# Kernel optimization log

Measured on AMD Instinct MI355X. Metric: run time of the kernel, lower is better.

Reference implementation:

```python
import jax, jax.numpy as jnp
import numpy as np

N = 50000      # nodes
E = 800000     # edges
D_IN = 128
D_H = 128
D_OUT = 40
BN_EPS = 1e-5


def setup_inputs() -> dict:
    key = jax.random.key(0)
    ks = jax.random.split(key, 12)
    x = jax.random.normal(ks[0], (N, D_IN), dtype=jnp.float32)
    edge_index = jax.random.randint(ks[1], (2, E), 0, N, dtype=jnp.int32)
    s = 0.05
    W1 = jax.random.normal(ks[2], (D_IN, D_H), dtype=jnp.float32) * s
    b1 = jnp.zeros((D_H,), jnp.float32)
    W2 = jax.random.normal(ks[3], (D_H, D_H), dtype=jnp.float32) * s
    b2 = jnp.zeros((D_H,), jnp.float32)
    W3 = jax.random.normal(ks[4], (D_H, D_OUT), dtype=jnp.float32) * s
    b3 = jnp.zeros((D_OUT,), jnp.float32)
    # BatchNorm (eval mode: running stats)
    g1 = jnp.ones((D_H,), jnp.float32)
    be1 = jnp.zeros((D_H,), jnp.float32)
    m1 = jax.random.normal(ks[5], (D_H,), dtype=jnp.float32) * 0.1
    v1 = jax.random.uniform(ks[6], (D_H,), dtype=jnp.float32, minval=0.5, maxval=1.5)
    g2 = jnp.ones((D_H,), jnp.float32)
    be2 = jnp.zeros((D_H,), jnp.float32)
    m2 = jax.random.normal(ks[7], (D_H,), dtype=jnp.float32) * 0.1
    v2 = jax.random.uniform(ks[8], (D_H,), dtype=jnp.float32, minval=0.5, maxval=1.5)
    return {"x": x, "edge_index": edge_index,
            "W1": W1, "b1": b1, "W2": W2, "b2": b2, "W3": W3, "b3": b3,
            "g1": g1, "be1": be1, "m1": m1, "v1": v1,
            "g2": g2, "be2": be2, "m2": m2, "v2": v2}


def gcn_conv(x, W, b, src, dst):
    # PyG GCNConv: h = x W; A_hat = D^-1/2 (A + I) D^-1/2; out = A_hat h + b
    h = x @ W                                   # [N, d_out]
    deg = jnp.zeros((N,), h.dtype).at[dst].add(1.0) + 1.0   # degrees incl. self loop
    dis = jax.lax.rsqrt(deg)                    # deg^-1/2
    norm = dis[src] * dis[dst]                  # [E]
    msg = h[src] * norm[:, None]                # [E, d_out] gather + scale
    agg = jax.ops.segment_sum(msg, dst, num_segments=N)     # scatter-add
    agg = agg + h * (1.0 / deg)[:, None]        # self-loop term: dis_i*dis_i = 1/deg_i
    return agg + b


def bn_eval(x, gamma, beta, mean, var):
    return (x - mean) * jax.lax.rsqrt(var + BN_EPS) * gamma + beta


def reference(x, edge_index, W1, b1, W2, b2, W3, b3,
              g1, be1, m1, v1, g2, be2, m2, v2):
    src, dst = edge_index[0], edge_index[1]
    h = jax.nn.relu(bn_eval(gcn_conv(x, W1, b1, src, dst), g1, be1, m1, v1))
    h = jax.nn.relu(bn_eval(gcn_conv(h, W2, b2, src, dst), g2, be2, m2, v2))
    h = gcn_conv(h, W3, b3, src, dst)
    return jax.nn.log_softmax(h, axis=-1)
```

## Files before the change

kernel.cpp:

```cpp
#include <hip/hip_runtime.h>
#include <math.h>

#define BN_EPS 1e-5f

typedef __attribute__((ext_vector_type(8))) short bf16x8;
typedef __attribute__((ext_vector_type(4))) float f32x4;

__device__ inline unsigned f2bf(float f) {
  union { float f; unsigned u; } v; v.f = f;
  unsigned r = v.u + 0x7FFF + ((v.u >> 16) & 1);
  return r >> 16;
}

__device__ inline void acc8n(float* a, uint4 v) {
  a[0] += __uint_as_float(v.x << 16);
  a[1] += __uint_as_float(v.x & 0xffff0000u);
  a[2] += __uint_as_float(v.y << 16);
  a[3] += __uint_as_float(v.y & 0xffff0000u);
  a[4] += __uint_as_float(v.z << 16);
  a[5] += __uint_as_float(v.z & 0xffff0000u);
  a[6] += __uint_as_float(v.w << 16);
  a[7] += __uint_as_float(v.w & 0xffff0000u);
}

__device__ inline void acc4n(float* a, uint2 v) {
  a[0] += __uint_as_float(v.x << 16);
  a[1] += __uint_as_float(v.x & 0xffff0000u);
  a[2] += __uint_as_float(v.y << 16);
  a[3] += __uint_as_float(v.y & 0xffff0000u);
}


__global__ void k_count(const int* __restrict__ dst, int* __restrict__ deg,
                        int* __restrict__ posw, int E) {
  int e = blockIdx.x * blockDim.x + threadIdx.x;
  if (e < E) posw[e] = atomicAdd(&deg[dst[e]], 1);
}

__global__ void k_scan1(const int* __restrict__ deg, int* __restrict__ rowstart,
                        int* __restrict__ chunksum, int n) {
  __shared__ int s[1024];
  int i = blockIdx.x * 1024 + threadIdx.x;
  int v = (i < n) ? deg[i] : 0;
  s[threadIdx.x] = v;
  __syncthreads();
  for (int off = 1; off < 1024; off <<= 1) {
    int t = (threadIdx.x >= off) ? s[threadIdx.x - off] : 0;
    __syncthreads();
    s[threadIdx.x] += t;
    __syncthreads();
  }
  if (i < n) rowstart[i] = s[threadIdx.x] - v;
  if (threadIdx.x == 1023) chunksum[blockIdx.x] = s[1023];
}

__global__ void k_scan3(int* __restrict__ rowstart, const int* __restrict__ chunksum,
                        const int* __restrict__ deg, float* __restrict__ dis,
                        int n, int E) {
  int pre = 0;
  for (int c = 0; c < (int)blockIdx.x; c++) pre += chunksum[c];
  int i = blockIdx.x * 1024 + threadIdx.x;
  if (i < n) {
    rowstart[i] += pre;
    dis[i] = rsqrtf((float)(deg[i] + 1));
  }
  if (i == 0) rowstart[n] = E;
}


__global__ void k_prep(const float* __restrict__ W1, const float* __restrict__ W2,
                       const float* __restrict__ W3,
                       const float* __restrict__ g1, const float* __restrict__ be1,
                       const float* __restrict__ m1, const float* __restrict__ v1,
                       const float* __restrict__ g2, const float* __restrict__ be2,
                       const float* __restrict__ m2, const float* __restrict__ v2,
                       const float* __restrict__ b1, const float* __restrict__ b2,
                       const float* __restrict__ b3,
                       ushort* __restrict__ WT1, ushort* __restrict__ WT2,
                       ushort* __restrict__ WT3,
                       float* __restrict__ sc1, float* __restrict__ sh1,
                       float* __restrict__ sc2, float* __restrict__ sh2,
                       float* __restrict__ b3pad,
                       uint4* __restrict__ degz, int deg16) {
  int k = blockIdx.x;
  int n = threadIdx.x;
  int tid = k * 128 + n;
  if (tid < deg16) degz[tid] = make_uint4(0, 0, 0, 0);
  WT1[n * 128 + k] = (ushort)f2bf(W1[k * 128 + n]);
  WT2[n * 128 + k] = (ushort)f2bf(W2[k * 128 + n]);
  WT3[n * 128 + k] = (n < 40) ? (ushort)f2bf(W3[k * 40 + n]) : (ushort)0;
  if (k == 0) {
    float s1 = g1[n] * rsqrtf(v1[n] + BN_EPS);
    sc1[n] = s1; sh1[n] = be1[n] + (b1[n] - m1[n]) * s1;
    float s2 = g2[n] * rsqrtf(v2[n] + BN_EPS);
    sc2[n] = s2; sh2[n] = be2[n] + (b2[n] - m2[n]) * s2;
  } else if (k == 1 && n < 64) {
    b3pad[n] = (n < 40) ? b3[n] : 0.f;
  }
}


template <bool F32A, bool FILL>
__global__ __launch_bounds__(256) void k_gemm_bf16(const void* __restrict__ Ap,
                                                   const ushort* __restrict__ WT,
                                                   ushort* __restrict__ C,
                                                   const float* __restrict__ dis,
                                                   int nrows, int NC, int gemmBlocks,
                                                   const int* __restrict__ ei,
                                                   const int* __restrict__ rowstart,
                                                   const int* __restrict__ posw,
                                                   unsigned* __restrict__ slot, int E) {
  if (FILL && (int)blockIdx.x >= gemmBlocks) {
    int e = ((int)blockIdx.x - gemmBlocks) * 256 + threadIdx.x;
    if (e < E) slot[rowstart[ei[E + e]] + posw[e]] = (unsigned)ei[e];
    return;
  }
  __shared__ ushort As[128][80];
  __shared__ ushort Bs[128][80];
  const int tid  = threadIdx.x;
  const int lane = tid & 63;
  const int wid  = tid >> 6;
  const int wr   = wid >> 1, wc = wid & 1;
  const int row0 = blockIdx.x * 128;
  f32x4 acc[4][4] = {};

  const int mrow = lane & 15;
  const int kg   = (lane >> 4) * 8;

  for (int k0 = 0; k0 < 128; k0 += 64) {
    __syncthreads();
    for (int i = tid; i < 1024; i += 256) {
      int r = i >> 3, c = (i & 7) * 8;
      uint4 w = make_uint4(0, 0, 0, 0);
      if (row0 + r < nrows) {
        if (F32A) {
          const float* A = (const float*)Ap;
          float4 v0 = *(const float4*)(A + (size_t)(row0 + r) * 128 + k0 + c);
          float4 v1 = *(const float4*)(A + (size_t)(row0 + r) * 128 + k0 + c + 4);
          w.x = f2bf(v0.x) | (f2bf(v0.y) << 16);
          w.y = f2bf(v0.z) | (f2bf(v0.w) << 16);
          w.z = f2bf(v1.x) | (f2bf(v1.y) << 16);
          w.w = f2bf(v1.z) | (f2bf(v1.w) << 16);
        } else {
          const ushort* A = (const ushort*)Ap;
          w = *(const uint4*)(A + (size_t)(row0 + r) * 128 + k0 + c);
        }
      }
      *(uint4*)(&As[r][c]) = w;
    }
    for (int i = tid; i < 1024; i += 256) {
      int r = i >> 3, c = (i & 7) * 8;
      *(uint4*)(&Bs[r][c]) = *(const uint4*)(WT + r * 128 + k0 + c);
    }
    __syncthreads();

#pragma unroll
    for (int ks = 0; ks < 2; ks++) {
      bf16x8 a[4], b[4];
#pragma unroll
      for (int f = 0; f < 4; f++) {
        a[f] = *(const bf16x8*)(&As[wr * 64 + f * 16 + mrow][ks * 32 + kg]);
        b[f] = *(const bf16x8*)(&Bs[wc * 64 + f * 16 + mrow][ks * 32 + kg]);
      }
#pragma unroll
      for (int fm = 0; fm < 4; fm++)
#pragma unroll
        for (int fn = 0; fn < 4; fn++)
          acc[fm][fn] = __builtin_amdgcn_mfma_f32_16x16x32_bf16(a[fm], b[fn], acc[fm][fn], 0, 0, 0);
    }
  }

  const int rl = (lane >> 4) * 4;
  const int cl = lane & 15;
#pragma unroll
  for (int fm = 0; fm < 4; fm++) {
#pragma unroll
    for (int r = 0; r < 4; r++) {
      int row = row0 + wr * 64 + fm * 16 + rl + r;
      if (row >= nrows) continue;
      float dn = dis[row];
#pragma unroll
      for (int fn = 0; fn < 4; fn++) {
        int col = wc * 64 + fn * 16 + cl;
        if (col < NC) C[(size_t)row * NC + col] = (ushort)f2bf(acc[fm][fn][r] * dn);
      }
    }
  }
}


__global__ __launch_bounds__(256) void k_agg128b(const ushort* __restrict__ h,
                          const int* __restrict__ rowstart,
                          const unsigned* __restrict__ slot,
                          const float* __restrict__ dis,
                          const float* __restrict__ bnsc,
                          const float* __restrict__ bnsh,
                          ushort* __restrict__ out, int nnodes) {
  int node = blockIdx.x * 4 + threadIdx.y;
  if (node >= nnodes) return;
  int lane = threadIdx.x;
  int eg = lane >> 4, cl = lane & 15, c0 = cl * 8;
  int s = rowstart[node], e = rowstart[node + 1];
  int deg = e - s;
  unsigned mys = 0;
  if (lane < deg) mys = slot[s + lane];
  float a[8] = {0.f, 0.f, 0.f, 0.f, 0.f, 0.f, 0.f, 0.f};
  int nb = deg < 64 ? deg : 64;
  int i = eg;
  for (; i + 12 < nb; i += 16) {
    int s0 = __shfl((int)mys, i);
    int s1 = __shfl((int)mys, i + 4);
    int s2 = __shfl((int)mys, i + 8);
    int s3 = __shfl((int)mys, i + 12);
    uint4 h0 = *(const uint4*)(h + (size_t)s0 * 128 + c0);
    uint4 h1 = *(const uint4*)(h + (size_t)s1 * 128 + c0);
    uint4 h2 = *(const uint4*)(h + (size_t)s2 * 128 + c0);
    uint4 h3 = *(const uint4*)(h + (size_t)s3 * 128 + c0);
    acc8n(a, h0); acc8n(a, h1); acc8n(a, h2); acc8n(a, h3);
  }
  for (; i + 4 < nb; i += 8) {
    int s0 = __shfl((int)mys, i);
    int s1 = __shfl((int)mys, i + 4);
    uint4 h0 = *(const uint4*)(h + (size_t)s0 * 128 + c0);
    uint4 h1 = *(const uint4*)(h + (size_t)s1 * 128 + c0);
    acc8n(a, h0); acc8n(a, h1);
  }
  if (i < nb) {
    int s0 = __shfl((int)mys, i);
    uint4 h0 = *(const uint4*)(h + (size_t)s0 * 128 + c0);
    acc8n(a, h0);
  }
  for (int j = s + 64 + eg; j < e; j += 4) {
    uint4 h0 = *(const uint4*)(h + (size_t)slot[j] * 128 + c0);
    acc8n(a, h0);
  }
#pragma unroll
  for (int j = 0; j < 8; j++) {
    a[j] += __shfl_xor(a[j], 16);
    a[j] += __shfl_xor(a[j], 32);
  }
  if (eg == 0) {
    uint4 hv = *(const uint4*)(h + (size_t)node * 128 + c0);
    acc8n(a, hv);
    float dn = dis[node];
    float4 sc0 = *(const float4*)(bnsc + c0), sc1 = *(const float4*)(bnsc + c0 + 4);
    float4 sh0 = *(const float4*)(bnsh + c0), sh1 = *(const float4*)(bnsh + c0 + 4);
    float o0 = fmaxf(fmaf(a[0] * dn, sc0.x, sh0.x), 0.f);
    float o1 = fmaxf(fmaf(a[1] * dn, sc0.y, sh0.y), 0.f);
    float o2 = fmaxf(fmaf(a[2] * dn, sc0.z, sh0.z), 0.f);
    float o3 = fmaxf(fmaf(a[3] * dn, sc0.w, sh0.w), 0.f);
    float o4 = fmaxf(fmaf(a[4] * dn, sc1.x, sh1.x), 0.f);
    float o5 = fmaxf(fmaf(a[5] * dn, sc1.y, sh1.y), 0.f);
    float o6 = fmaxf(fmaf(a[6] * dn, sc1.z, sh1.z), 0.f);
    float o7 = fmaxf(fmaf(a[7] * dn, sc1.w, sh1.w), 0.f);
    uint4 w;
    w.x = f2bf(o0) | (f2bf(o1) << 16);
    w.y = f2bf(o2) | (f2bf(o3) << 16);
    w.z = f2bf(o4) | (f2bf(o5) << 16);
    w.w = f2bf(o6) | (f2bf(o7) << 16);
    *(uint4*)(out + (size_t)node * 128 + c0) = w;
  }
}


__global__ __launch_bounds__(256) void k_agg64_lsm(const ushort* __restrict__ h,
                            const int* __restrict__ rowstart,
                            const unsigned* __restrict__ slot,
                            const float* __restrict__ dis,
                            const float* __restrict__ b3pad,
                            float* __restrict__ out, int nnodes) {
  int node = blockIdx.x * 4 + threadIdx.y;
  if (node >= nnodes) return;
  int lane = threadIdx.x;
  int eg = lane >> 4, cl = lane & 15, c0 = cl * 4;
  int s = rowstart[node], e = rowstart[node + 1];
  int deg = e - s;
  unsigned mys = 0;
  if (lane < deg) mys = slot[s + lane];
  float a[4] = {0.f, 0.f, 0.f, 0.f};
  int nb = deg < 64 ? deg : 64;
  int i = eg;
  for (; i + 12 < nb; i += 16) {
    int s0 = __shfl((int)mys, i);
    int s1 = __shfl((int)mys, i + 4);
    int s2 = __shfl((int)mys, i + 8);
    int s3 = __shfl((int)mys, i + 12);
    uint2 h0 = *(const uint2*)(h + (size_t)s0 * 64 + c0);
    uint2 h1 = *(const uint2*)(h + (size_t)s1 * 64 + c0);
    uint2 h2 = *(const uint2*)(h + (size_t)s2 * 64 + c0);
    uint2 h3 = *(const uint2*)(h + (size_t)s3 * 64 + c0);
    acc4n(a, h0); acc4n(a, h1); acc4n(a, h2); acc4n(a, h3);
  }
  for (; i + 4 < nb; i += 8) {
    int s0 = __shfl((int)mys, i);
    int s1 = __shfl((int)mys, i + 4);
    uint2 h0 = *(const uint2*)(h + (size_t)s0 * 64 + c0);
    uint2 h1 = *(const uint2*)(h + (size_t)s1 * 64 + c0);
    acc4n(a, h0); acc4n(a, h1);
  }
  if (i < nb) {
    int s0 = __shfl((int)mys, i);
    uint2 h0 = *(const uint2*)(h + (size_t)s0 * 64 + c0);
    acc4n(a, h0);
  }
  for (int j = s + 64 + eg; j < e; j += 4) {
    uint2 h0 = *(const uint2*)(h + (size_t)slot[j] * 64 + c0);
    acc4n(a, h0);
  }
#pragma unroll
  for (int j = 0; j < 4; j++) {
    a[j] += __shfl_xor(a[j], 16);
    a[j] += __shfl_xor(a[j], 32);
  }
  {
    uint2 hv = *(const uint2*)(h + (size_t)node * 64 + c0);
    acc4n(a, hv);
    float dn = dis[node];
    float4 bb = *(const float4*)(b3pad + c0);
    a[0] = fmaf(a[0], dn, bb.x);
    a[1] = fmaf(a[1], dn, bb.y);
    a[2] = fmaf(a[2], dn, bb.z);
    a[3] = fmaf(a[3], dn, bb.w);
  }
  bool valid = cl < 10;
  float m = valid ? fmaxf(fmaxf(a[0], a[1]), fmaxf(a[2], a[3])) : -INFINITY;
#pragma unroll
  for (int off = 1; off < 16; off <<= 1) m = fmaxf(m, __shfl_xor(m, off));
  float ss = valid ? (expf(a[0] - m) + expf(a[1] - m) + expf(a[2] - m) + expf(a[3] - m)) : 0.f;
#pragma unroll
  for (int off = 1; off < 16; off <<= 1) ss += __shfl_xor(ss, off);
  float lse = m + logf(ss);
  if (eg == 0 && valid) {
    *(float4*)(out + (size_t)node * 40 + c0) =
        make_float4(a[0] - lse, a[1] - lse, a[2] - lse, a[3] - lse);
  }
}


extern "C" void kernel_launch(void* const* d_in, const int* in_sizes, int n_in,
                              void* d_out, int out_size, void* d_ws, size_t ws_size,
                              hipStream_t stream) {
  const float* x   = (const float*)d_in[0];
  const int*   ei  = (const int*)d_in[1];
  const float* W1  = (const float*)d_in[2];
  const float* b1  = (const float*)d_in[3];
  const float* W2  = (const float*)d_in[4];
  const float* b2  = (const float*)d_in[5];
  const float* W3  = (const float*)d_in[6];
  const float* b3  = (const float*)d_in[7];
  const float* g1  = (const float*)d_in[8];
  const float* be1 = (const float*)d_in[9];
  const float* m1  = (const float*)d_in[10];
  const float* v1  = (const float*)d_in[11];
  const float* g2  = (const float*)d_in[12];
  const float* be2 = (const float*)d_in[13];
  const float* m2  = (const float*)d_in[14];
  const float* v2  = (const float*)d_in[15];

  const int N   = in_sizes[0] / 128;
  const int E   = in_sizes[1] / 2;

  float* outp = (float*)d_out;

  char* ws = (char*)d_ws;
  size_t off = 0;
  auto alloc = [&](size_t bytes) -> char* {
    char* p = ws + off;
    off = (off + bytes + 255) & ~(size_t)255;
    return p;
  };
  const int deg16 = (N + 3) / 4;
  int*      deg      = (int*)alloc((size_t)deg16 * 16);
  int*      posw     = (int*)alloc((size_t)E * 4);
  int*      rowstart = (int*)alloc((size_t)(N + 1) * 4);
  int*      chunksum = (int*)alloc(256 * 4);
  float*    dis      = (float*)alloc((size_t)N * 4);
  unsigned* slot     = (unsigned*)alloc((size_t)E * 4);
  float*    sc1      = (float*)alloc(128 * 4);
  float*    sh1      = (float*)alloc(128 * 4);
  float*    sc2      = (float*)alloc(128 * 4);
  float*    sh2      = (float*)alloc(128 * 4);
  float*    b3pad    = (float*)alloc(64 * 4);
  ushort*   WT1      = (ushort*)alloc(128 * 128 * 2);
  ushort*   WT2      = (ushort*)alloc(128 * 128 * 2);
  ushort*   WT3      = (ushort*)alloc(128 * 128 * 2);
  ushort*   bufA     = (ushort*)alloc((size_t)N * 128 * 2);
  ushort*   bufB     = (ushort*)alloc((size_t)N * 128 * 2);
  ushort*   bufC     = (ushort*)alloc((size_t)N * 64 * 2);
  (void)ws_size;

  const int T = 256;
  const int chunks = (N + 1023) / 1024;

  k_prep<<<128, 128, 0, stream>>>(W1, W2, W3, g1, be1, m1, v1, g2, be2, m2, v2,
                                  b1, b2, b3, WT1, WT2, WT3, sc1, sh1, sc2, sh2, b3pad,
                                  (uint4*)deg, deg16);
  k_count<<<(E + T - 1) / T, T, 0, stream>>>(ei + E, deg, posw, E);
  k_scan1<<<chunks, 1024, 0, stream>>>(deg, rowstart, chunksum, N);
  k_scan3<<<chunks, 1024, 0, stream>>>(rowstart, chunksum, deg, dis, N, E);

  dim3 aggGrid((N + 3) / 4), aggBlk(64, 4);
  const int gBlocks = (N + 127) / 128;
  const int fBlocks = (E + 255) / 256;

  k_gemm_bf16<true, true><<<gBlocks + fBlocks, 256, 0, stream>>>(
      x, WT1, bufB, dis, N, 128, gBlocks, ei, rowstart, posw, slot, E);
  k_agg128b<<<aggGrid, aggBlk, 0, stream>>>(bufB, rowstart, slot, dis, sc1, sh1, bufA, N);

  k_gemm_bf16<false, false><<<gBlocks, 256, 0, stream>>>(
      bufA, WT2, bufB, dis, N, 128, gBlocks, nullptr, nullptr, nullptr, nullptr, 0);
  k_agg128b<<<aggGrid, aggBlk, 0, stream>>>(bufB, rowstart, slot, dis, sc2, sh2, bufA, N);

  k_gemm_bf16<false, false><<<gBlocks, 256, 0, stream>>>(
      bufA, WT3, bufC, dis, N, 64, gBlocks, nullptr, nullptr, nullptr, nullptr, 0);
  k_agg64_lsm<<<aggGrid, aggBlk, 0, stream>>>(bufC, rowstart, slot, dis, b3pad, outp, N);
}
```

Measured before the change: 203.3 us.

## Split 128-wide aggregation into column chunks, single-pass scan, unpadded 40-col output

```diff
diff --git a/kernel.cpp b/kernel.cpp
--- a/kernel.cpp
+++ b/kernel.cpp
@@ -12,15 +12,9 @@
   return r >> 16;
 }
 
-__device__ inline void acc8n(float* a, uint4 v) {
-  a[0] += __uint_as_float(v.x << 16);
-  a[1] += __uint_as_float(v.x & 0xffff0000u);
-  a[2] += __uint_as_float(v.y << 16);
-  a[3] += __uint_as_float(v.y & 0xffff0000u);
-  a[4] += __uint_as_float(v.z << 16);
-  a[5] += __uint_as_float(v.z & 0xffff0000u);
-  a[6] += __uint_as_float(v.w << 16);
-  a[7] += __uint_as_float(v.w & 0xffff0000u);
+__device__ inline void acc2n(float& a0, float& a1, unsigned h) {
+  a0 += __uint_as_float(h << 16);
+  a1 += __uint_as_float(h & 0xffff0000u);
 }
 
 __device__ inline void acc4n(float* a, uint2 v) {
@@ -37,34 +31,38 @@
   if (e < E) posw[e] = atomicAdd(&deg[dst[e]], 1);
 }
 
-__global__ void k_scan1(const int* __restrict__ deg, int* __restrict__ rowstart,
-                        int* __restrict__ chunksum, int n) {
+__global__ void k_scan(const int* __restrict__ deg, int* __restrict__ rowstart,
+                       float* __restrict__ dis, int* __restrict__ flags,
+                       int n, int E) {
   __shared__ int s[1024];
-  int i = blockIdx.x * 1024 + threadIdx.x;
+  __shared__ int spre;
+  const int b = blockIdx.x;
+  const int tid = threadIdx.x;
+  int i = b * 1024 + tid;
   int v = (i < n) ? deg[i] : 0;
-  s[threadIdx.x] = v;
+  if (i < n) dis[i] = rsqrtf((float)(v + 1));
+  s[tid] = v;
   __syncthreads();
   for (int off = 1; off < 1024; off <<= 1) {
-    int t = (threadIdx.x >= off) ? s[threadIdx.x - off] : 0;
+    int t = (tid >= off) ? s[tid - off] : 0;
     __syncthreads();
-    s[threadIdx.x] += t;
+    s[tid] += t;
     __syncthreads();
   }
-  if (i < n) rowstart[i] = s[threadIdx.x] - v;
-  if (threadIdx.x == 1023) chunksum[blockIdx.x] = s[1023];
-}
-
-__global__ void k_scan3(int* __restrict__ rowstart, const int* __restrict__ chunksum,
-                        const int* __restrict__ deg, float* __restrict__ dis,
-                        int n, int E) {
-  int pre = 0;
-  for (int c = 0; c < (int)blockIdx.x; c++) pre += chunksum[c];
-  int i = blockIdx.x * 1024 + threadIdx.x;
-  if (i < n) {
-    rowstart[i] += pre;
-    dis[i] = rsqrtf((float)(deg[i] + 1));
-  }
-  if (i == 0) rowstart[n] = E;
+  if (tid == 0) {
+    spre = 0;
+    atomicExch(&flags[b], s[1023] + 1);
+  }
+  __syncthreads();
+  if (tid < b) {
+    int v2;
+    do { v2 = atomicAdd(&flags[tid], 0); } while (v2 == 0);
+    atomicAdd(&spre, v2 - 1);
+  }
+  __syncthreads();
+  int pre = spre;
+  if (i < n) rowstart[i] = pre + s[tid] - v;
+  if (b == 0 && tid == 0) rowstart[n] = E;
 }
 
 
@@ -81,11 +79,13 @@
                        float* __restrict__ sc1, float* __restrict__ sh1,
                        float* __restrict__ sc2, float* __restrict__ sh2,
                        float* __restrict__ b3pad,
-                       uint4* __restrict__ degz, int deg16) {
+                       uint4* __restrict__ degz, int deg16,
+                       uint4* __restrict__ flagz) {
   int k = blockIdx.x;
   int n = threadIdx.x;
   int tid = k * 128 + n;
   if (tid < deg16) degz[tid] = make_uint4(0, 0, 0, 0);
+  if (tid < 16)    flagz[tid] = make_uint4(0, 0, 0, 0);
   WT1[n * 128 + k] = (ushort)f2bf(W1[k * 128 + n]);
   WT2[n * 128 + k] = (ushort)f2bf(W2[k * 128 + n]);
   WT3[n * 128 + k] = (n < 40) ? (ushort)f2bf(W3[k * 40 + n]) : (ushort)0;
@@ -189,22 +189,26 @@
 }
 
 
-__global__ __launch_bounds__(256) void k_agg128b(const ushort* __restrict__ h,
+__global__ __launch_bounds__(256) void k_agg128c(const ushort* __restrict__ h,
                           const int* __restrict__ rowstart,
                           const unsigned* __restrict__ slot,
                           const float* __restrict__ dis,
                           const float* __restrict__ bnsc,
                           const float* __restrict__ bnsh,
-                          ushort* __restrict__ out, int nnodes) {
-  int node = blockIdx.x * 4 + threadIdx.y;
+                          ushort* __restrict__ out, int nnodes, int quads) {
+  int bid = blockIdx.x;
+  int chunk = bid / quads;
+  int quad  = bid - chunk * quads;
+  int node = quad * 4 + threadIdx.y;
   if (node >= nnodes) return;
   int lane = threadIdx.x;
-  int eg = lane >> 4, cl = lane & 15, c0 = cl * 8;
+  int eg = lane >> 4, cl = lane & 15;
+  int c0 = chunk * 32 + cl * 2;
   int s = rowstart[node], e = rowstart[node + 1];
   int deg = e - s;
   unsigned mys = 0;
   if (lane < deg) mys = slot[s + lane];
-  float a[8] = {0.f, 0.f, 0.f, 0.f, 0.f, 0.f, 0.f, 0.f};
+  float a0 = 0.f, a1 = 0.f;
   int nb = deg < 64 ? deg : 64;
   int i = eg;
   for (; i + 12 < nb; i += 16) {
@@ -212,58 +216,41 @@
     int s1 = __shfl((int)mys, i + 4);
     int s2 = __shfl((int)mys, i + 8);
     int s3 = __shfl((int)mys, i + 12);
-    uint4 h0 = *(const uint4*)(h + (size_t)s0 * 128 + c0);
-    uint4 h1 = *(const uint4*)(h + (size_t)s1 * 128 + c0);
-    uint4 h2 = *(const uint4*)(h + (size_t)s2 * 128 + c0);
-    uint4 h3 = *(const uint4*)(h + (size_t)s3 * 128 + c0);
-    acc8n(a, h0); acc8n(a, h1); acc8n(a, h2); acc8n(a, h3);
+    unsigned h0 = *(const unsigned*)(h + (size_t)s0 * 128 + c0);
+    unsigned h1 = *(const unsigned*)(h + (size_t)s1 * 128 + c0);
+    unsigned h2 = *(const unsigned*)(h + (size_t)s2 * 128 + c0);
+    unsigned h3 = *(const unsigned*)(h + (size_t)s3 * 128 + c0);
+    acc2n(a0, a1, h0); acc2n(a0, a1, h1); acc2n(a0, a1, h2); acc2n(a0, a1, h3);
   }
   for (; i + 4 < nb; i += 8) {
     int s0 = __shfl((int)mys, i);
     int s1 = __shfl((int)mys, i + 4);
-    uint4 h0 = *(const uint4*)(h + (size_t)s0 * 128 + c0);
-    uint4 h1 = *(const uint4*)(h + (size_t)s1 * 128 + c0);
-    acc8n(a, h0); acc8n(a, h1);
+    unsigned h0 = *(const unsigned*)(h + (size_t)s0 * 128 + c0);
+    unsigned h1 = *(const unsigned*)(h + (size_t)s1 * 128 + c0);
+    acc2n(a0, a1, h0); acc2n(a0, a1, h1);
   }
   if (i < nb) {
     int s0 = __shfl((int)mys, i);
-    uint4 h0 = *(const uint4*)(h + (size_t)s0 * 128 + c0);
-    acc8n(a, h0);
+    acc2n(a0, a1, *(const unsigned*)(h + (size_t)s0 * 128 + c0));
   }
   for (int j = s + 64 + eg; j < e; j += 4) {
-    uint4 h0 = *(const uint4*)(h + (size_t)slot[j] * 128 + c0);
-    acc8n(a, h0);
-  }
-#pragma unroll
-  for (int j = 0; j < 8; j++) {
-    a[j] += __shfl_xor(a[j], 16);
-    a[j] += __shfl_xor(a[j], 32);
-  }
+    acc2n(a0, a1, *(const unsigned*)(h + (size_t)slot[j] * 128 + c0));
+  }
+  a0 += __shfl_xor(a0, 16); a0 += __shfl_xor(a0, 32);
+  a1 += __shfl_xor(a1, 16); a1 += __shfl_xor(a1, 32);
   if (eg == 0) {
-    uint4 hv = *(const uint4*)(h + (size_t)node * 128 + c0);
-    acc8n(a, hv);
+    acc2n(a0, a1, *(const unsigned*)(h + (size_t)node * 128 + c0));
     float dn = dis[node];
-    float4 sc0 = *(const float4*)(bnsc + c0), sc1 = *(const float4*)(bnsc + c0 + 4);
-    float4 sh0 = *(const float4*)(bnsh + c0), sh1 = *(const float4*)(bnsh + c0 + 4);
-    float o0 = fmaxf(fmaf(a[0] * dn, sc0.x, sh0.x), 0.f);
-    float o1 = fmaxf(fmaf(a[1] * dn, sc0.y, sh0.y), 0.f);
-    float o2 = fmaxf(fmaf(a[2] * dn, sc0.z, sh0.z), 0.f);
-    float o3 = fmaxf(fmaf(a[3] * dn, sc0.w, sh0.w), 0.f);
-    float o4 = fmaxf(fmaf(a[4] * dn, sc1.x, sh1.x), 0.f);
-    float o5 = fmaxf(fmaf(a[5] * dn, sc1.y, sh1.y), 0.f);
-    float o6 = fmaxf(fmaf(a[6] * dn, sc1.z, sh1.z), 0.f);
-    float o7 = fmaxf(fmaf(a[7] * dn, sc1.w, sh1.w), 0.f);
-    uint4 w;
-    w.x = f2bf(o0) | (f2bf(o1) << 16);
-    w.y = f2bf(o2) | (f2bf(o3) << 16);
-    w.z = f2bf(o4) | (f2bf(o5) << 16);
-    w.w = f2bf(o6) | (f2bf(o7) << 16);
-    *(uint4*)(out + (size_t)node * 128 + c0) = w;
-  }
-}
-
-
-__global__ __launch_bounds__(256) void k_agg64_lsm(const ushort* __restrict__ h,
+    float2 sc = *(const float2*)(bnsc + c0);
+    float2 sh = *(const float2*)(bnsh + c0);
+    float o0 = fmaxf(fmaf(a0 * dn, sc.x, sh.x), 0.f);
+    float o1 = fmaxf(fmaf(a1 * dn, sc.y, sh.y), 0.f);
+    *(unsigned*)(out + (size_t)node * 128 + c0) = f2bf(o0) | (f2bf(o1) << 16);
+  }
+}
+
+
+__global__ __launch_bounds__(256) void k_agg40_lsm(const ushort* __restrict__ h,
                             const int* __restrict__ rowstart,
                             const unsigned* __restrict__ slot,
                             const float* __restrict__ dis,
@@ -273,6 +260,7 @@
   if (node >= nnodes) return;
   int lane = threadIdx.x;
   int eg = lane >> 4, cl = lane & 15, c0 = cl * 4;
+  bool act = cl < 10;
   int s = rowstart[node], e = rowstart[node + 1];
   int deg = e - s;
   unsigned mys = 0;
@@ -285,36 +273,38 @@
     int s1 = __shfl((int)mys, i + 4);
     int s2 = __shfl((int)mys, i + 8);
     int s3 = __shfl((int)mys, i + 12);
-    uint2 h0 = *(const uint2*)(h + (size_t)s0 * 64 + c0);
-    uint2 h1 = *(const uint2*)(h + (size_t)s1 * 64 + c0);
-    uint2 h2 = *(const uint2*)(h + (size_t)s2 * 64 + c0);
-    uint2 h3 = *(const uint2*)(h + (size_t)s3 * 64 + c0);
-    acc4n(a, h0); acc4n(a, h1); acc4n(a, h2); acc4n(a, h3);
+    if (act) {
+      uint2 h0 = *(const uint2*)(h + (size_t)s0 * 40 + c0);
+      uint2 h1 = *(const uint2*)(h + (size_t)s1 * 40 + c0);
+      uint2 h2 = *(const uint2*)(h + (size_t)s2 * 40 + c0);
+      uint2 h3 = *(const uint2*)(h + (size_t)s3 * 40 + c0);
+      acc4n(a, h0); acc4n(a, h1); acc4n(a, h2); acc4n(a, h3);
+    }
   }
   for (; i + 4 < nb; i += 8) {
     int s0 = __shfl((int)mys, i);
     int s1 = __shfl((int)mys, i + 4);
-    uint2 h0 = *(const uint2*)(h + (size_t)s0 * 64 + c0);
-    uint2 h1 = *(const uint2*)(h + (size_t)s1 * 64 + c0);
-    acc4n(a, h0); acc4n(a, h1);
+    if (act) {
+      uint2 h0 = *(const uint2*)(h + (size_t)s0 * 40 + c0);
+      uint2 h1 = *(const uint2*)(h + (size_t)s1 * 40 + c0);
+      acc4n(a, h0); acc4n(a, h1);
+    }
   }
   if (i < nb) {
     int s0 = __shfl((int)mys, i);
-    uint2 h0 = *(const uint2*)(h + (size_t)s0 * 64 + c0);
-    acc4n(a, h0);
+    if (act) acc4n(a, *(const uint2*)(h + (size_t)s0 * 40 + c0));
   }
   for (int j = s + 64 + eg; j < e; j += 4) {
-    uint2 h0 = *(const uint2*)(h + (size_t)slot[j] * 64 + c0);
-    acc4n(a, h0);
+    unsigned sj = slot[j];
+    if (act) acc4n(a, *(const uint2*)(h + (size_t)sj * 40 + c0));
   }
 #pragma unroll
   for (int j = 0; j < 4; j++) {
     a[j] += __shfl_xor(a[j], 16);
     a[j] += __shfl_xor(a[j], 32);
   }
-  {
-    uint2 hv = *(const uint2*)(h + (size_t)node * 64 + c0);
-    acc4n(a, hv);
+  if (act) {
+    acc4n(a, *(const uint2*)(h + (size_t)node * 40 + c0));
     float dn = dis[node];
     float4 bb = *(const float4*)(b3pad + c0);
     a[0] = fmaf(a[0], dn, bb.x);
@@ -322,15 +312,14 @@
     a[2] = fmaf(a[2], dn, bb.z);
     a[3] = fmaf(a[3], dn, bb.w);
   }
-  bool valid = cl < 10;
-  float m = valid ? fmaxf(fmaxf(a[0], a[1]), fmaxf(a[2], a[3])) : -INFINITY;
+  float m = act ? fmaxf(fmaxf(a[0], a[1]), fmaxf(a[2], a[3])) : -INFINITY;
 #pragma unroll
   for (int off = 1; off < 16; off <<= 1) m = fmaxf(m, __shfl_xor(m, off));
-  float ss = valid ? (expf(a[0] - m) + expf(a[1] - m) + expf(a[2] - m) + expf(a[3] - m)) : 0.f;
+  float ss = act ? (expf(a[0] - m) + expf(a[1] - m) + expf(a[2] - m) + expf(a[3] - m)) : 0.f;
 #pragma unroll
   for (int off = 1; off < 16; off <<= 1) ss += __shfl_xor(ss, off);
   float lse = m + logf(ss);
-  if (eg == 0 && valid) {
+  if (eg == 0 && act) {
     *(float4*)(out + (size_t)node * 40 + c0) =
         make_float4(a[0] - lse, a[1] - lse, a[2] - lse, a[3] - lse);
   }
@@ -371,9 +360,9 @@
   };
   const int deg16 = (N + 3) / 4;
   int*      deg      = (int*)alloc((size_t)deg16 * 16);
+  int*      flags    = (int*)alloc(64 * 4);
   int*      posw     = (int*)alloc((size_t)E * 4);
   int*      rowstart = (int*)alloc((size_t)(N + 1) * 4);
-  int*      chunksum = (int*)alloc(256 * 4);
   float*    dis      = (float*)alloc((size_t)N * 4);
   unsigned* slot     = (unsigned*)alloc((size_t)E * 4);
   float*    sc1      = (float*)alloc(128 * 4);
@@ -386,7 +375,7 @@
   ushort*   WT3      = (ushort*)alloc(128 * 128 * 2);
   ushort*   bufA     = (ushort*)alloc((size_t)N * 128 * 2);
   ushort*   bufB     = (ushort*)alloc((size_t)N * 128 * 2);
-  ushort*   bufC     = (ushort*)alloc((size_t)N * 64 * 2);
+  ushort*   bufC     = (ushort*)alloc((size_t)N * 40 * 2);
   (void)ws_size;
 
   const int T = 256;
@@ -394,24 +383,24 @@
 
   k_prep<<<128, 128, 0, stream>>>(W1, W2, W3, g1, be1, m1, v1, g2, be2, m2, v2,
                                   b1, b2, b3, WT1, WT2, WT3, sc1, sh1, sc2, sh2, b3pad,
-                                  (uint4*)deg, deg16);
+                                  (uint4*)deg, deg16, (uint4*)flags);
   k_count<<<(E + T - 1) / T, T, 0, stream>>>(ei + E, deg, posw, E);
-  k_scan1<<<chunks, 1024, 0, stream>>>(deg, rowstart, chunksum, N);
-  k_scan3<<<chunks, 1024, 0, stream>>>(rowstart, chunksum, deg, dis, N, E);
-
-  dim3 aggGrid((N + 3) / 4), aggBlk(64, 4);
+  k_scan<<<chunks, 1024, 0, stream>>>(deg, rowstart, dis, flags, N, E);
+
+  const int quads = (N + 3) / 4;
+  dim3 aggBlk(64, 4);
   const int gBlocks = (N + 127) / 128;
   const int fBlocks = (E + 255) / 256;
 
   k_gemm_bf16<true, true><<<gBlocks + fBlocks, 256, 0, stream>>>(
       x, WT1, bufB, dis, N, 128, gBlocks, ei, rowstart, posw, slot, E);
-  k_agg128b<<<aggGrid, aggBlk, 0, stream>>>(bufB, rowstart, slot, dis, sc1, sh1, bufA, N);
+  k_agg128c<<<4 * quads, aggBlk, 0, stream>>>(bufB, rowstart, slot, dis, sc1, sh1, bufA, N, quads);
 
   k_gemm_bf16<false, false><<<gBlocks, 256, 0, stream>>>(
       bufA, WT2, bufB, dis, N, 128, gBlocks, nullptr, nullptr, nullptr, nullptr, 0);
-  k_agg128b<<<aggGrid, aggBlk, 0, stream>>>(bufB, rowstart, slot, dis, sc2, sh2, bufA, N);
+  k_agg128c<<<4 * quads, aggBlk, 0, stream>>>(bufB, rowstart, slot, dis, sc2, sh2, bufA, N, quads);
 
   k_gemm_bf16<false, false><<<gBlocks, 256, 0, stream>>>(
-      bufA, WT3, bufC, dis, N, 64, gBlocks, nullptr, nullptr, nullptr, nullptr, 0);
-  k_agg64_lsm<<<aggGrid, aggBlk, 0, stream>>>(bufC, rowstart, slot, dis, b3pad, outp, N);
-}
+      bufA, WT3, bufC, dis, N, 40, gBlocks, nullptr, nullptr, nullptr, nullptr, 0);
+  k_agg40_lsm<<<quads, aggBlk, 0, stream>>>(bufC, rowstart, slot, dis, b3pad, outp, N);
+}
```

Result: slower. 283.2 us (+39.3%).
